# Optimization experiments

Measured on AMD Instinct MI355X. Metric: run time of the kernel, lower is better.

## Reference

```python
import jax, jax.numpy as jnp
import numpy as np

# Model constants (solved parameter set; precip and water_efficiency from source)
TS = 0.0001
PRECIP = 1.845
WATER_EFFICIENCY = 0.449
SEEP_RATE = 0.2
UPTAKE_RATE = 1.0
ETA = 3.0
Q = 1.0
MORT_RATE = 0.3
D2 = 1.0
D3 = 0.05


def laplacian(x):
    # 3x3 5-point Laplacian stencil with replicate (edge) padding, x: [B,1,H,W]
    xp = jnp.pad(x, ((0, 0), (0, 0), (1, 1), (1, 1)), mode='edge')
    return (xp[:, :, :-2, 1:-1] + xp[:, :, 2:, 1:-1]
            + xp[:, :, 1:-1, :-2] + xp[:, :, 1:-1, 2:] - 4.0 * x)


def setup_inputs() -> dict:
    key = jax.random.key(0)
    k1, k2, k3 = jax.random.split(key, 3)
    shape = (16, 1, 1024, 1024)
    w = jax.random.uniform(k1, shape, dtype=jnp.float32)
    b = jax.random.uniform(k2, shape, dtype=jnp.float32)
    T = jax.random.uniform(k3, shape, dtype=jnp.float32)
    return {"w": w, "b": b, "T": T}


def reference(w, b, T):
    uptake = UPTAKE_RATE * w * b * (1.0 + ETA * b ** Q)
    dw = (D2 * laplacian(w) - SEEP_RATE * w + PRECIP - uptake) * TS
    db = (D3 * laplacian(b) - MORT_RATE * T * b + WATER_EFFICIENCY * uptake) * TS
    return (w + dw, b + db)
```

## Files before the change

### kernel.cpp

```cpp
#include <hip/hip_runtime.h>


namespace {
constexpr int IMGS = 16;
constexpr int H = 1024;
constexpr int W = 1024;
constexpr size_t PLANE = (size_t)H * W;
constexpr int RPB = 4;
}

typedef float f4 __attribute__((ext_vector_type(4)));

__global__ __launch_bounds__(256) void nca_step(
    const float* __restrict__ wg, const float* __restrict__ bg,
    const float* __restrict__ Tg, float* __restrict__ owg,
    float* __restrict__ obg)
{
    const int nwg = gridDim.x;
    const int cpx = nwg >> 3;
    const int bid = blockIdx.x;
    const int swz = (bid & 7) * cpx + (bid >> 3);

    const int img = swz >> 8;
    const int r0  = (swz & 255) * RPB;
    const int t    = threadIdx.x;
    const int lane = t & 63;
    const int x0   = t << 2;

    const float* wp = wg + (size_t)img * PLANE;
    const float* bp = bg + (size_t)img * PLANE;
    const float* Tp = Tg + (size_t)img * PLANE;

    const int rm1 = (r0 > 0)       ? r0 - 1   : 0;
    const int rp4 = (r0 + RPB < H) ? r0 + RPB : H - 1;

    f4 wv[RPB + 2], bv[RPB + 2], Tv[RPB];
    wv[0] = *(const f4*)(wp + (size_t)rm1 * W + x0);
    bv[0] = *(const f4*)(bp + (size_t)rm1 * W + x0);
#pragma unroll
    for (int i = 0; i < RPB; ++i) {
        wv[i + 1] = *(const f4*)(wp + (size_t)(r0 + i) * W + x0);
        bv[i + 1] = *(const f4*)(bp + (size_t)(r0 + i) * W + x0);
        Tv[i] = __builtin_nontemporal_load((const f4*)(Tp + (size_t)(r0 + i) * W + x0));
    }
    wv[RPB + 1] = *(const f4*)(wp + (size_t)rp4 * W + x0);
    bv[RPB + 1] = *(const f4*)(bp + (size_t)rp4 * W + x0);

#pragma unroll
    for (int i = 0; i < RPB; ++i) {
        const f4 cw = wv[i + 1], uw = wv[i], dw = wv[i + 2];
        const f4 cb = bv[i + 1], ub = bv[i], db = bv[i + 2];
        const f4 cT = Tv[i];

        float wl = __shfl_up(cw.w, 1);
        float wr = __shfl_down(cw.x, 1);
        float bl = __shfl_up(cb.w, 1);
        float br = __shfl_down(cb.x, 1);
        const float* wrow = wp + (size_t)(r0 + i) * W;
        const float* brow = bp + (size_t)(r0 + i) * W;
        if (lane == 0) {
            wl = (x0 > 0) ? wrow[x0 - 1] : cw.x;
            bl = (x0 > 0) ? brow[x0 - 1] : cb.x;
        }
        if (lane == 63) {
            wr = (x0 + 4 < W) ? wrow[x0 + 4] : cw.w;
            br = (x0 + 4 < W) ? brow[x0 + 4] : cb.w;
        }

        f4 lw, lb;
        lw.x = uw.x + dw.x + wl   + cw.y - 4.0f * cw.x;
        lw.y = uw.y + dw.y + cw.x + cw.z - 4.0f * cw.y;
        lw.z = uw.z + dw.z + cw.y + cw.w - 4.0f * cw.z;
        lw.w = uw.w + dw.w + cw.z + wr   - 4.0f * cw.w;

        lb.x = ub.x + db.x + bl   + cb.y - 4.0f * cb.x;
        lb.y = ub.y + db.y + cb.x + cb.z - 4.0f * cb.y;
        lb.z = ub.z + db.z + cb.y + cb.w - 4.0f * cb.z;
        lb.w = ub.w + db.w + cb.z + br   - 4.0f * cb.w;

        f4 ow4, ob4;
#pragma unroll
        for (int j = 0; j < 4; ++j) {
            const float up = cw[j] * cb[j] * (1.0f + 3.0f * cb[j]);
            ow4[j] = cw[j] + (lw[j] - 0.2f * cw[j] + 1.845f - up) * 1e-4f;
            ob4[j] = cb[j] + (0.05f * lb[j] - 0.3f * cT[j] * cb[j] + 0.449f * up) * 1e-4f;
        }

        const size_t oidx = (size_t)img * PLANE + (size_t)(r0 + i) * W + x0;
        __builtin_nontemporal_store(ow4, (f4*)(owg + oidx));
        __builtin_nontemporal_store(ob4, (f4*)(obg + oidx));
    }
}

extern "C" void kernel_launch(void* const* d_in, const int* in_sizes, int n_in,
                              void* d_out, int out_size, void* d_ws, size_t ws_size,
                              hipStream_t stream) {
    const float* w = (const float*)d_in[0];
    const float* b = (const float*)d_in[1];
    const float* T = (const float*)d_in[2];
    float* ow = (float*)d_out;
    float* ob = ow + (size_t)IMGS * PLANE;

    dim3 grid(IMGS * (H / RPB));
    dim3 block(W / 4);
    nca_step<<<grid, block, 0, stream>>>(w, b, T, ow, ob);
}
```

Measured before the change: 284.7 us.

## Stream 16-row strips with register rolling window and software-prefetched next rows

Each block now handles 16 rows instead of 4. It walks down them two rows at a time, keeping a rolling register window of w and b rows and prefetching the next pair (plus T and the halo edge values) before computing the current pair. A sched_barrier keeps the prefetch loads issued ahead of the compute. This cuts halo row re-reads from 6/4 to 18/16 and overlaps memory latency with compute. The cost is fewer blocks, so less parallelism, and more registers per thread, with launch bounds set to 4 blocks per CU.

```diff
diff --git a/kernel.cpp b/kernel.cpp
--- a/kernel.cpp
+++ b/kernel.cpp
@@ -6,12 +6,45 @@
 constexpr int H = 1024;
 constexpr int W = 1024;
 constexpr size_t PLANE = (size_t)H * W;
-constexpr int RPB = 4;
+constexpr int RPB = 16;
+constexpr int NT  = 8;
 }
 
 typedef float f4 __attribute__((ext_vector_type(4)));
 
-__global__ __launch_bounds__(256) void nca_step(
+__device__ __forceinline__ void row_update(
+    const f4 uw, const f4 cw, const f4 dw,
+    const f4 ub, const f4 cb, const f4 db,
+    const f4 cT, float elW, float erW, float elB, float erB,
+    int lane, int x0, f4& ow4, f4& ob4)
+{
+    float wl = __shfl_up(cw.w, 1);
+    float wr = __shfl_down(cw.x, 1);
+    float bl = __shfl_up(cb.w, 1);
+    float br = __shfl_down(cb.x, 1);
+    if (lane == 0)  { wl = (x0 > 0)     ? elW : cw.x;  bl = (x0 > 0)     ? elB : cb.x; }
+    if (lane == 63) { wr = (x0 + 4 < W) ? erW : cw.w;  br = (x0 + 4 < W) ? erB : cb.w; }
+
+    f4 lw, lb;
+    lw.x = uw.x + dw.x + wl   + cw.y - 4.0f * cw.x;
+    lw.y = uw.y + dw.y + cw.x + cw.z - 4.0f * cw.y;
+    lw.z = uw.z + dw.z + cw.y + cw.w - 4.0f * cw.z;
+    lw.w = uw.w + dw.w + cw.z + wr   - 4.0f * cw.w;
+
+    lb.x = ub.x + db.x + bl   + cb.y - 4.0f * cb.x;
+    lb.y = ub.y + db.y + cb.x + cb.z - 4.0f * cb.y;
+    lb.z = ub.z + db.z + cb.y + cb.w - 4.0f * cb.z;
+    lb.w = ub.w + db.w + cb.z + br   - 4.0f * cb.w;
+
+#pragma unroll
+    for (int j = 0; j < 4; ++j) {
+        const float up = cw[j] * cb[j] * (1.0f + 3.0f * cb[j]);
+        ow4[j] = cw[j] + (lw[j] - 0.2f * cw[j] + 1.845f - up) * 1e-4f;
+        ob4[j] = cb[j] + (0.05f * lb[j] - 0.3f * cT[j] * cb[j] + 0.449f * up) * 1e-4f;
+    }
+}
+
+__global__ __launch_bounds__(256, 4) void nca_step(
     const float* __restrict__ wg, const float* __restrict__ bg,
     const float* __restrict__ Tg, float* __restrict__ owg,
     float* __restrict__ obg)
@@ -21,8 +54,8 @@
     const int bid = blockIdx.x;
     const int swz = (bid & 7) * cpx + (bid >> 3);
 
-    const int img = swz >> 8;
-    const int r0  = (swz & 255) * RPB;
+    const int img = swz >> 6;
+    const int rs  = (swz & 63) * RPB;
     const int t    = threadIdx.x;
     const int lane = t & 63;
     const int x0   = t << 2;
@@ -30,65 +63,80 @@
     const float* wp = wg + (size_t)img * PLANE;
     const float* bp = bg + (size_t)img * PLANE;
     const float* Tp = Tg + (size_t)img * PLANE;
+    float* owp = owg + (size_t)img * PLANE;
+    float* obp = obg + (size_t)img * PLANE;
 
-    const int rm1 = (r0 > 0)       ? r0 - 1   : 0;
-    const int rp4 = (r0 + RPB < H) ? r0 + RPB : H - 1;
+    const bool pL = (lane == 0)  && (x0 > 0);
+    const bool pR = (lane == 63) && (x0 + 4 < W);
 
-    f4 wv[RPB + 2], bv[RPB + 2], Tv[RPB];
-    wv[0] = *(const f4*)(wp + (size_t)rm1 * W + x0);
-    bv[0] = *(const f4*)(bp + (size_t)rm1 * W + x0);
-#pragma unroll
-    for (int i = 0; i < RPB; ++i) {
-        wv[i + 1] = *(const f4*)(wp + (size_t)(r0 + i) * W + x0);
-        bv[i + 1] = *(const f4*)(bp + (size_t)(r0 + i) * W + x0);
-        Tv[i] = __builtin_nontemporal_load((const f4*)(Tp + (size_t)(r0 + i) * W + x0));
-    }
-    wv[RPB + 1] = *(const f4*)(wp + (size_t)rp4 * W + x0);
-    bv[RPB + 1] = *(const f4*)(bp + (size_t)rp4 * W + x0);
+    const int rm = (rs > 0) ? rs - 1 : 0;
+    f4 wv0 = *(const f4*)(wp + (size_t)rm * W + x0);
+    f4 wv1 = *(const f4*)(wp + (size_t)rs * W + x0);
+    f4 wv2 = *(const f4*)(wp + (size_t)(rs + 1) * W + x0);
+    f4 wv3 = *(const f4*)(wp + (size_t)(rs + 2) * W + x0);
+    f4 bv0 = *(const f4*)(bp + (size_t)rm * W + x0);
+    f4 bv1 = *(const f4*)(bp + (size_t)rs * W + x0);
+    f4 bv2 = *(const f4*)(bp + (size_t)(rs + 1) * W + x0);
+    f4 bv3 = *(const f4*)(bp + (size_t)(rs + 2) * W + x0);
+    f4 tv0 = __builtin_nontemporal_load((const f4*)(Tp + (size_t)rs * W + x0));
+    f4 tv1 = __builtin_nontemporal_load((const f4*)(Tp + (size_t)(rs + 1) * W + x0));
+
+    float eWl0 = pL ? wp[(size_t)rs * W + x0 - 1]       : 0.0f;
+    float eWl1 = pL ? wp[(size_t)(rs + 1) * W + x0 - 1] : 0.0f;
+    float eWr0 = pR ? wp[(size_t)rs * W + x0 + 4]       : 0.0f;
+    float eWr1 = pR ? wp[(size_t)(rs + 1) * W + x0 + 4] : 0.0f;
+    float eBl0 = pL ? bp[(size_t)rs * W + x0 - 1]       : 0.0f;
+    float eBl1 = pL ? bp[(size_t)(rs + 1) * W + x0 - 1] : 0.0f;
+    float eBr0 = pR ? bp[(size_t)rs * W + x0 + 4]       : 0.0f;
+    float eBr1 = pR ? bp[(size_t)(rs + 1) * W + x0 + 4] : 0.0f;
 
 #pragma unroll
-    for (int i = 0; i < RPB; ++i) {
-        const f4 cw = wv[i + 1], uw = wv[i], dw = wv[i + 2];
-        const f4 cb = bv[i + 1], ub = bv[i], db = bv[i + 2];
-        const f4 cT = Tv[i];
+    for (int it = 0; it < NT; ++it) {
+        const int r0 = rs + it * 2;
 
-        float wl = __shfl_up(cw.w, 1);
-        float wr = __shfl_down(cw.x, 1);
-        float bl = __shfl_up(cb.w, 1);
-        float br = __shfl_down(cb.x, 1);
-        const float* wrow = wp + (size_t)(r0 + i) * W;
-        const float* brow = bp + (size_t)(r0 + i) * W;
-        if (lane == 0) {
-            wl = (x0 > 0) ? wrow[x0 - 1] : cw.x;
-            bl = (x0 > 0) ? brow[x0 - 1] : cb.x;
-        }
-        if (lane == 63) {
-            wr = (x0 + 4 < W) ? wrow[x0 + 4] : cw.w;
-            br = (x0 + 4 < W) ? brow[x0 + 4] : cb.w;
+        f4 nw0, nw1, nb0, nb1, nt0, nt1;
+        float nWl0 = 0.0f, nWl1 = 0.0f, nWr0 = 0.0f, nWr1 = 0.0f;
+        float nBl0 = 0.0f, nBl1 = 0.0f, nBr0 = 0.0f, nBr1 = 0.0f;
+        if (it < NT - 1) {
+            const int ra = r0 + 3;
+            const int rb = (r0 + 4 < H) ? (r0 + 4) : (H - 1);
+            nw0 = *(const f4*)(wp + (size_t)ra * W + x0);
+            nw1 = *(const f4*)(wp + (size_t)rb * W + x0);
+            nb0 = *(const f4*)(bp + (size_t)ra * W + x0);
+            nb1 = *(const f4*)(bp + (size_t)rb * W + x0);
+            nt0 = __builtin_nontemporal_load((const f4*)(Tp + (size_t)(r0 + 2) * W + x0));
+            nt1 = __builtin_nontemporal_load((const f4*)(Tp + (size_t)(r0 + 3) * W + x0));
+            nWl0 = pL ? wp[(size_t)(r0 + 2) * W + x0 - 1] : 0.0f;
+            nWl1 = pL ? wp[(size_t)(r0 + 3) * W + x0 - 1] : 0.0f;
+            nWr0 = pR ? wp[(size_t)(r0 + 2) * W + x0 + 4] : 0.0f;
+            nWr1 = pR ? wp[(size_t)(r0 + 3) * W + x0 + 4] : 0.0f;
+            nBl0 = pL ? bp[(size_t)(r0 + 2) * W + x0 - 1] : 0.0f;
+            nBl1 = pL ? bp[(size_t)(r0 + 3) * W + x0 - 1] : 0.0f;
+            nBr0 = pR ? bp[(size_t)(r0 + 2) * W + x0 + 4] : 0.0f;
+            nBr1 = pR ? bp[(size_t)(r0 + 3) * W + x0 + 4] : 0.0f;
         }
 
-        f4 lw, lb;
-        lw.x = uw.x + dw.x + wl   + cw.y - 4.0f * cw.x;
-        lw.y = uw.y + dw.y + cw.x + cw.z - 4.0f * cw.y;
-        lw.z = uw.z + dw.z + cw.y + cw.w - 4.0f * cw.z;
-        lw.w = uw.w + dw.w + cw.z + wr   - 4.0f * cw.w;
+        __builtin_amdgcn_sched_barrier(0);
 
-        lb.x = ub.x + db.x + bl   + cb.y - 4.0f * cb.x;
-        lb.y = ub.y + db.y + cb.x + cb.z - 4.0f * cb.y;
-        lb.z = ub.z + db.z + cb.y + cb.w - 4.0f * cb.z;
-        lb.w = ub.w + db.w + cb.z + br   - 4.0f * cb.w;
+        f4 ow0, ob0, ow1, ob1;
+        row_update(wv0, wv1, wv2, bv0, bv1, bv2, tv0,
+                   eWl0, eWr0, eBl0, eBr0, lane, x0, ow0, ob0);
+        row_update(wv1, wv2, wv3, bv1, bv2, bv3, tv1,
+                   eWl1, eWr1, eBl1, eBr1, lane, x0, ow1, ob1);
 
-        f4 ow4, ob4;
-#pragma unroll
-        for (int j = 0; j < 4; ++j) {
-            const float up = cw[j] * cb[j] * (1.0f + 3.0f * cb[j]);
-            ow4[j] = cw[j] + (lw[j] - 0.2f * cw[j] + 1.845f - up) * 1e-4f;
-            ob4[j] = cb[j] + (0.05f * lb[j] - 0.3f * cT[j] * cb[j] + 0.449f * up) * 1e-4f;
+        const size_t o0 = (size_t)r0 * W + x0;
+        __builtin_nontemporal_store(ow0, (f4*)(owp + o0));
+        __builtin_nontemporal_store(ob0, (f4*)(obp + o0));
+        __builtin_nontemporal_store(ow1, (f4*)(owp + o0 + W));
+        __builtin_nontemporal_store(ob1, (f4*)(obp + o0 + W));
+
+        if (it < NT - 1) {
+            wv0 = wv2; wv1 = wv3; wv2 = nw0; wv3 = nw1;
+            bv0 = bv2; bv1 = bv3; bv2 = nb0; bv3 = nb1;
+            tv0 = nt0; tv1 = nt1;
+            eWl0 = nWl0; eWl1 = nWl1; eWr0 = nWr0; eWr1 = nWr1;
+            eBl0 = nBl0; eBl1 = nBl1; eBr0 = nBr0; eBr1 = nBr1;
         }
-
-        const size_t oidx = (size_t)img * PLANE + (size_t)(r0 + i) * W + x0;
-        __builtin_nontemporal_store(ow4, (f4*)(owg + oidx));
-        __builtin_nontemporal_store(ob4, (f4*)(obg + oidx));
     }
 }
 
```

Measured after the change: 289.0 us. Within noise of the previous version (+1.5%).
